# Performance work log

Measured on AMD Instinct MI355X. Metric: run time of the kernel, lower is better.

The kernel has to match this reference:

```python
import jax, jax.numpy as jnp
import numpy as np

B, S, D, H, FFN = 8, 1024, 1024, 16, 4096
DH = D // H  # per-head dim = 64
NEG = -1e9
EPS = 1e-5


def layer_norm(x):
    # F.layer_norm over last dim, no affine params (matches add_and_norm_dropout)
    mu = jnp.mean(x, axis=-1, keepdims=True)
    var = jnp.var(x, axis=-1, keepdims=True)
    return (x - mu) / jnp.sqrt(var + EPS)


def setup_inputs() -> dict:
    key = jax.random.key(0)
    ks = jax.random.split(key, 10)
    scale = 1.0 / np.sqrt(D)
    x = jax.random.normal(ks[0], (B, S, D), dtype=jnp.float32)
    real_lengths = jax.random.randint(ks[1], (B,), 1, S + 1)
    # per-head projection weights stacked: [H, D, DH] (nn.Linear(D, DH, bias=False) per head)
    Wq = jax.random.uniform(ks[2], (H, D, DH), jnp.float32, -scale, scale)
    Wk = jax.random.uniform(ks[3], (H, D, DH), jnp.float32, -scale, scale)
    Wv = jax.random.uniform(ks[4], (H, D, DH), jnp.float32, -scale, scale)
    Wo = jax.random.uniform(ks[5], (D, H * DH), jnp.float32, -scale, scale)  # Linear(H*DH, D, bias=False)
    W1 = jax.random.uniform(ks[6], (FFN, D), jnp.float32, -scale, scale)
    b1 = jax.random.uniform(ks[7], (FFN,), jnp.float32, -scale, scale)
    s2 = 1.0 / np.sqrt(FFN)
    W2 = jax.random.uniform(ks[8], (D, FFN), jnp.float32, -s2, s2)
    b2 = jax.random.uniform(ks[9], (D,), jnp.float32, -s2, s2)
    return {"x": x, "real_lengths": real_lengths, "Wq": Wq, "Wk": Wk, "Wv": Wv,
            "Wo": Wo, "W1": W1, "b1": b1, "W2": W2, "b2": b2}


def reference(x, real_lengths, Wq, Wk, Wv, Wo, W1, b1, W2, b2):
    b, s, d = x.shape
    # padding mask: True where key position >= real_length (masked out)
    key_pad = jnp.arange(s)[None, :] >= real_lengths[:, None]  # [B, S]

    # batched per-head projections (equivalent to the Python per-head loop)
    q = jnp.einsum('bsd,hde->bhse', x, Wq)
    k = jnp.einsum('bsd,hde->bhse', x, Wk)
    v = jnp.einsum('bsd,hde->bhse', x, Wv)

    scores = jnp.einsum('bhse,bhte->bhst', q, k) / jnp.sqrt(jnp.float32(DH))
    scores = jnp.where(key_pad[:, None, None, :], NEG, scores)
    attn = jax.nn.softmax(scores, axis=-1)
    heads = jnp.einsum('bhst,bhte->bhse', attn, v)       # [B,H,S,DH]
    concat = heads.transpose(0, 2, 1, 3).reshape(b, s, d)  # head concat
    attn_out = concat @ Wo.T

    x1 = layer_norm(x + attn_out)  # add & norm (eval: no dropout)

    ffn = jax.nn.relu(x1 @ W1.T + b1) @ W2.T + b2
    return layer_norm(x1 + ffn)
```

## Files before the change

### kernel.cpp

```cpp
#include <hip/hip_runtime.h>
#include <hip/hip_bf16.h>
#include <math.h>

#define B_ 8
#define S_ 1024
#define D_ 1024
#define H_ 16
#define DH_ 64
#define FFN_ 4096
#define NEG_ (-1e9f)
#define EPS_ 1e-5f

typedef float f32x4 __attribute__((ext_vector_type(4)));
typedef short bf16x8 __attribute__((ext_vector_type(8)));

__device__ __forceinline__ ushort f2b(float f) {
  __hip_bfloat16 h = __float2bfloat16(f);
  return *reinterpret_cast<ushort*>(&h);
}
__device__ __forceinline__ float b2f(ushort u) {
  return __uint_as_float((unsigned)u << 16);
}

__device__ __forceinline__ void gload16(const void* g, void* l) {
  auto* lp = (__attribute__((address_space(3))) unsigned*)(uintptr_t)(l);
  __builtin_amdgcn_global_load_lds(
      (const __attribute__((address_space(1))) unsigned*)g, lp, 16, 0, 0);
}

__device__ __forceinline__ void* swz_ptr(void* base, int row, int col) {
  int byte = (row << 7) + (col << 1);
  byte ^= (row & 7) << 4;
  return (char*)base + byte;
}
__device__ __forceinline__ void* swz256(void* base, int row, int col) {
  int byte = (row << 8) + (col << 1);
  byte ^= (row & 7) << 4;
  return (char*)base + byte;
}

#define BARR asm volatile("s_barrier" ::: "memory")
#define LGKM0                                         \
  do {                                                \
    asm volatile("s_waitcnt lgkmcnt(0)" ::: "memory"); \
    __builtin_amdgcn_sched_barrier(0);                \
  } while (0)

__global__ __launch_bounds__(256) void prep_k(
    const float* __restrict__ x, const float* __restrict__ Wq,
    const float* __restrict__ Wk, const float* __restrict__ Wv,
    const float* __restrict__ Wo, const float* __restrict__ W1,
    const float* __restrict__ W2, ushort* __restrict__ xbf,
    ushort* __restrict__ qkvw, ushort* __restrict__ wob,
    ushort* __restrict__ w1b, ushort* __restrict__ w2b) {
  const int blk = blockIdx.x, t = threadIdx.x;
  if (blk < 8192) {
    int i = blk * 256 + t;
    float4 v = ((const float4*)x)[i];
    ushort4 o;
    o.x = f2b(v.x); o.y = f2b(v.y); o.z = f2b(v.z); o.w = f2b(v.w);
    ((ushort4*)xbf)[i] = o;
  } else if (blk < 8192 + 12288) {
    int idx = (blk - 8192) * 256 + t;
    int k = idx & 1023, e = (idx >> 10) & 63;
    int h = (idx >> 16) & 15, which = idx >> 20;
    const float* W = (which == 0) ? Wq : (which == 1 ? Wk : Wv);
    float v = W[((size_t)h * D_ + k) * DH_ + e];
    qkvw[((size_t)which * 1024 + h * 64 + e) * 1024 + k] = f2b(v);
  } else if (blk < 8192 + 12288 + 1024) {
    int i = (blk - 8192 - 12288) * 256 + t;
    float4 v = ((const float4*)Wo)[i];
    ushort4 o;
    o.x = f2b(v.x); o.y = f2b(v.y); o.z = f2b(v.z); o.w = f2b(v.w);
    ((ushort4*)wob)[i] = o;
  } else if (blk < 8192 + 12288 + 1024 + 4096) {
    int i = (blk - 8192 - 12288 - 1024) * 256 + t;
    float4 v = ((const float4*)W1)[i];
    ushort4 o;
    o.x = f2b(v.x); o.y = f2b(v.y); o.z = f2b(v.z); o.w = f2b(v.w);
    ((ushort4*)w1b)[i] = o;
  } else {
    int i = (blk - 8192 - 12288 - 1024 - 4096) * 256 + t;
    float4 v = ((const float4*)W2)[i];
    ushort4 o;
    o.x = f2b(v.x); o.y = f2b(v.y); o.z = f2b(v.z); o.w = f2b(v.w);
    ((ushort4*)w2b)[i] = o;
  }
}

template <int BIAS, int RELU, int VSPLIT, int SPLITK>
__global__ __launch_bounds__(512, 2) void gemm8p(
    const ushort* __restrict__ A, const ushort* __restrict__ Bt,
    const float* __restrict__ bias, ushort* __restrict__ C,
    ushort* __restrict__ C2, int M, int N, int K) {
  __shared__ ushort lds[2][2][2][256 * 32];
  int bid = blockIdx.x;
  int nwg = gridDim.x;
  int kh2 = 0;
  if (SPLITK) {
    int hw = nwg >> 1;
    if (bid >= hw) { kh2 = 1; bid -= hw; }
    nwg = hw;
  }
  const int nbn = N >> 8;
  const int cpx = nwg >> 3;
  const int swz = (bid & 7) * cpx + (bid >> 3);
  const int bm = swz / nbn, bn = swz % nbn;
  const int Keff = SPLITK ? (K >> 1) : K;

  const int t = threadIdx.x;
  const int lane = t & 63, lr = lane & 15, lg = lane >> 4;
  const int wid = t >> 6, wr = wid >> 2, wc = wid & 3;
  const size_t Kb = (size_t)K * 2;
  const char* Ab = (const char*)A + ((size_t)(bm << 8)) * Kb +
                   (size_t)kh2 * Keff * 2;
  const char* Bb = (const char*)Bt + ((size_t)(bn << 8)) * Kb +
                   (size_t)kh2 * Keff * 2;
  const int NT = Keff >> 6;
  const int niter = NT >> 1;

  const int g0row = t >> 2;
  const int gsi = (t & 3) ^ ((g0row >> 2) & 3);
  auto STG = [&](int mat, int kh, int kt) {
    char* base = (char*)&lds[kt & 1][mat][kh][0];
    const char* gsrc = mat ? Bb : Ab;
#pragma unroll
    for (int j = 0; j < 2; j++) {
      int row = g0row + j * 128;
      const char* src = gsrc + (size_t)row * Kb +
                        (size_t)(kt * 64 + kh * 32) * 2 + gsi * 16;
      gload16(src, base + t * 16 + j * 8192);
    }
  };

  const int rg = (lg ^ ((lr >> 2) & 3)) << 3;
#define LDA(DST, BUF, KH, QM)                                            \
  _Pragma("unroll") for (int mm = 0; mm < 4; mm++) {                     \
    int row = wr * 128 + (QM)*64 + mm * 16 + lr;                         \
    DST[mm] = *(const bf16x8*)&lds[BUF][0][KH][row * 32 + rg];           \
  }
#define LDB(DST, BUF, KH)                                                \
  _Pragma("unroll") for (int nn = 0; nn < 4; nn++) {                     \
    int row = wc * 64 + nn * 16 + lr;                                    \
    DST[nn] = *(const bf16x8*)&lds[BUF][1][KH][row * 32 + rg];           \
  }
#define MFQ(QM, AS, BS)                                                  \
  do {                                                                   \
    __builtin_amdgcn_s_setprio(1);                                       \
    _Pragma("unroll") for (int mm = 0; mm < 4; mm++)                     \
        _Pragma("unroll") for (int nn = 0; nn < 4; nn++)                 \
            acc[(QM)*4 + mm][nn] = __builtin_amdgcn_mfma_f32_16x16x32_bf16( \
                AS[mm], BS[nn], acc[(QM)*4 + mm][nn], 0, 0, 0);          \
    __builtin_amdgcn_s_setprio(0);                                       \
  } while (0)

  f32x4 acc[8][4] = {};
  bf16x8 aS0[4], aS1[4], bS0[4], bS1[4];

  STG(0, 0, 0); STG(1, 0, 0); STG(0, 1, 0); STG(1, 1, 0);
  STG(0, 0, 1); STG(1, 0, 1);
  asm volatile("s_waitcnt vmcnt(4)" ::: "memory");
  BARR;

  for (int i = 0; i < niter; i++) {
    const int c1 = 2 * i + 1, c2 = 2 * i + 2, c3 = 2 * i + 3;
    LDA(aS0, 0, 0, 0); LDB(bS0, 0, 0); STG(0, 1, c1);
    BARR; LGKM0; MFQ(0, aS0, bS0); BARR;
    LDA(aS1, 0, 0, 1); STG(1, 1, c1);
    BARR; LGKM0; MFQ(1, aS1, bS0); BARR;
    LDA(aS0, 0, 1, 0); LDB(bS1, 0, 1);
    if (c2 < NT) STG(0, 0, c2);
    BARR; LGKM0; MFQ(0, aS0, bS1); BARR;
    LDA(aS1, 0, 1, 1);
    if (c2 < NT) STG(1, 0, c2);
    BARR; LGKM0; MFQ(1, aS1, bS1);
    if (i + 1 < niter)
      asm volatile("s_waitcnt vmcnt(4)" ::: "memory");
    else
      asm volatile("s_waitcnt vmcnt(0)" ::: "memory");
    BARR;
    LDA(aS0, 1, 0, 0); LDB(bS0, 1, 0);
    if (c2 < NT) STG(0, 1, c2);
    BARR; LGKM0; MFQ(0, aS0, bS0); BARR;
    LDA(aS1, 1, 0, 1);
    if (c2 < NT) STG(1, 1, c2);
    BARR; LGKM0; MFQ(1, aS1, bS0); BARR;
    LDA(aS0, 1, 1, 0); LDB(bS1, 1, 1);
    if (c3 < NT) STG(0, 0, c3);
    BARR; LGKM0; MFQ(0, aS0, bS1); BARR;
    LDA(aS1, 1, 1, 1);
    if (c3 < NT) STG(1, 0, c3);
    BARR; LGKM0; MFQ(1, aS1, bS1);
    asm volatile("s_waitcnt vmcnt(4)" ::: "memory");
    BARR;
  }
#undef LDA
#undef LDB
#undef MFQ

  ushort* Cout = (SPLITK && kh2) ? C2 : C;
  const int addb = BIAS && !(SPLITK && kh2);
  const int r0 = (bm << 8) + wr * 128 + lg * 4;
  const int c0 = (bn << 8) + wc * 64 + lr;
#pragma unroll
  for (int m = 0; m < 8; m++) {
#pragma unroll
    for (int n = 0; n < 4; n++) {
      int col = c0 + n * 16;
      float bv = addb ? bias[col] : 0.0f;
      if (VSPLIT && col >= 2048) {
        int row = r0 + m * 16;
        int hh = (col - 2048) >> 6, e = col & 63;
        ushort4 uv;
        uv.x = f2b(acc[m][n][0]); uv.y = f2b(acc[m][n][1]);
        uv.z = f2b(acc[m][n][2]); uv.w = f2b(acc[m][n][3]);
        *(ushort4*)&C2[((((size_t)(row >> 10) * 16 + hh) * 64 + e) << 10) +
                       (row & 1023)] = uv;
      } else {
#pragma unroll
        for (int q = 0; q < 4; q++) {
          int row = r0 + m * 16 + q;
          float v = acc[m][n][q] + bv;
          if (RELU) v = fmaxf(v, 0.0f);
          if (VSPLIT)
            Cout[(size_t)row * 2048 + col] = f2b(v);
          else
            Cout[(size_t)row * N + col] = f2b(v);
        }
      }
    }
  }
}

__global__ __launch_bounds__(256) void attention_mfma_k(
    const ushort* __restrict__ qk, const ushort* __restrict__ vT,
    const int* __restrict__ lens, ushort* __restrict__ concat) {
  __shared__ ushort Qs[64 * 64];
  __shared__ ushort Ks[128 * 64];
  __shared__ ushort Vt[64 * 128];
  __shared__ ushort Pl[4][16 * 128];
  const int blk = blockIdx.x;
  int lv[8];
#pragma unroll
  for (int j = 0; j < 8; j++) lv[j] = lens[j];
  const int rank = blk >> 8;
  int b = 0;
#pragma unroll
  for (int cand = 0; cand < 8; cand++) {
    int r = 0;
#pragma unroll
    for (int j = 0; j < 8; j++)
      r += (lv[j] > lv[cand]) || (lv[j] == lv[cand] && j < cand);
    if (r == rank) b = cand;
  }
  const int h = (blk >> 4) & 15, q0 = (blk & 15) << 6;
  const int t = threadIdx.x;
  const int lane = t & 63, w = t >> 6;
  const int lr = lane & 15, lg = lane >> 4;
  const int lg4 = lg * 4;
  const int len_b = lv[b];
  ushort* Plw = &Pl[w][0];
  const ushort* vbase = vT + ((size_t)(b * 16 + h) << 16);

#pragma unroll
  for (int i = 0; i < 4; i++) {
    int idx = t + i * 256;
    int r = idx >> 4, eq = idx & 15;
    const ushort* src =
        qk + ((size_t)(b * S_ + q0 + r)) * 2048 + h * 64 + eq * 4;
    *(ushort4*)swz_ptr(Qs, r, eq * 4) = *(const ushort4*)src;
  }
  __syncthreads();
  bf16x8 qf[2];
#pragma unroll
  for (int ds = 0; ds < 2; ds++)
    qf[ds] = *(const bf16x8*)swz_ptr(Qs, w * 16 + lr, lg * 8 + ds * 32);

  float mrun = -INFINITY, lrun = 0.f;
  f32x4 o[4] = {};

  ushort4 kreg[8], vreg[8];
  auto LOADT = [&](int j0) {
#pragma unroll
    for (int i = 0; i < 8; i++) {
      int idx = t + i * 256;
      int kr = idx >> 4, keq = idx & 15;
      kreg[i] = *(const ushort4*)(qk + ((size_t)(b * S_ + j0 + kr)) * 2048 +
                                  1024 + h * 64 + keq * 4);
      int vr = idx >> 5, vc = idx & 31;
      vreg[i] = *(const ushort4*)(vbase + (size_t)vr * 1024 + j0 + vc * 4);
    }
  };

  const int ntiles = (len_b + 127) >> 7;
  LOADT(0);
  for (int jt = 0; jt < ntiles; jt++) {
    const int j0 = jt << 7;
    __syncthreads();
#pragma unroll
    for (int i = 0; i < 8; i++) {
      int idx = t + i * 256;
      int kr = idx >> 4, keq = idx & 15;
      *(ushort4*)swz_ptr(Ks, kr, keq * 4) = kreg[i];
      int vr = idx >> 5, vc = idx & 31;
      *(ushort4*)swz256(Vt, vr, vc * 4) = vreg[i];
    }
    if (jt + 1 < ntiles) LOADT(j0 + 128);
    __syncthreads();

    f32x4 sacc[8];
    __builtin_amdgcn_s_setprio(1);
#pragma unroll
    for (int mb = 0; mb < 8; mb++) {
      sacc[mb] = (f32x4){0.f, 0.f, 0.f, 0.f};
#pragma unroll
      for (int ds = 0; ds < 2; ds++) {
        bf16x8 kf = *(const bf16x8*)swz_ptr(Ks, mb * 16 + lr, lg * 8 + ds * 32);
        sacc[mb] = __builtin_amdgcn_mfma_f32_16x16x32_bf16(kf, qf[ds], sacc[mb],
                                                           0, 0, 0);
      }
    }
    __builtin_amdgcn_s_setprio(0);

    float p[8][4];
    float pmax = -INFINITY;
#pragma unroll
    for (int mb = 0; mb < 8; mb++)
#pragma unroll
      for (int qi = 0; qi < 4; qi++) {
        float v = sacc[mb][qi] * 0.125f;
        if (j0 + mb * 16 + lg4 + qi >= len_b) v = NEG_;
        p[mb][qi] = v;
        pmax = fmaxf(pmax, v);
      }
    pmax = fmaxf(pmax, __shfl_xor(pmax, 16));
    pmax = fmaxf(pmax, __shfl_xor(pmax, 32));
    if (!__all(pmax - mrun <= 8.0f)) {
      float mnew = fmaxf(mrun, pmax);
      float sc = __expf(mrun - mnew);
      mrun = mnew;
      lrun *= sc;
#pragma unroll
      for (int qi = 0; qi < 4; qi++) {
        float scq = __shfl(sc, (lg << 4) + lg4 + qi);
#pragma unroll
        for (int dt = 0; dt < 4; dt++) o[dt][qi] *= scq;
      }
    }
    float rs = 0.f;
#pragma unroll
    for (int mb = 0; mb < 8; mb++)
#pragma unroll
      for (int qi = 0; qi < 4; qi++) {
        float e = __expf(p[mb][qi] - mrun);
        p[mb][qi] = e;
        rs += e;
      }
    rs += __shfl_xor(rs, 16);
    rs += __shfl_xor(rs, 32);
    lrun += rs;

#pragma unroll
    for (int mb = 0; mb < 8; mb++) {
      ushort2 w0, w1;
      w0.x = f2b(p[mb][0]); w0.y = f2b(p[mb][1]);
      w1.x = f2b(p[mb][2]); w1.y = f2b(p[mb][3]);
      *(ushort2*)swz256(Plw, lr, mb * 16 + lg4) = w0;
      *(ushort2*)swz256(Plw, lr, mb * 16 + lg4 + 2) = w1;
    }

    bf16x8 pf[4];
#pragma unroll
    for (int ks = 0; ks < 4; ks++)
      pf[ks] = *(const bf16x8*)swz256(Plw, lr, lg * 8 + ks * 32);
    __builtin_amdgcn_s_setprio(1);
#pragma unroll
    for (int dt = 0; dt < 4; dt++) {
#pragma unroll
      for (int ks = 0; ks < 4; ks++) {
        bf16x8 vf =
            *(const bf16x8*)swz256(Vt, dt * 16 + lr, ks * 32 + lg * 8);
        o[dt] = __builtin_amdgcn_mfma_f32_16x16x32_bf16(pf[ks], vf, o[dt],
                                                        0, 0, 0);
      }
    }
    __builtin_amdgcn_s_setprio(0);
  }

#pragma unroll
  for (int qi = 0; qi < 4; qi++) {
    float lq = __shfl(lrun, (lg << 4) + lg4 + qi);
    float inv = 1.0f / lq;
    size_t row = (size_t)(b * S_ + q0 + w * 16 + lg4 + qi);
#pragma unroll
    for (int dt = 0; dt < 4; dt++)
      concat[row * 1024 + h * 64 + dt * 16 + lr] = f2b(o[dt][qi] * inv);
  }
}

template <int WY, int WBF, int TWO, int ABF>
__global__ __launch_bounds__(256) void add_ln_k(const void* __restrict__ a,
                                                const ushort* __restrict__ r,
                                                const ushort* __restrict__ r2,
                                                float* __restrict__ y,
                                                ushort* __restrict__ yb) {
  const int row = blockIdx.x, t = threadIdx.x;
  float v[4];
  if (ABF) {
    const ushort4 av = ((const ushort4*)((const ushort*)a + (size_t)row * 1024))[t];
    v[0] = b2f(av.x); v[1] = b2f(av.y); v[2] = b2f(av.z); v[3] = b2f(av.w);
  } else {
    const float4 av = ((const float4*)((const float*)a + (size_t)row * 1024))[t];
    v[0] = av.x; v[1] = av.y; v[2] = av.z; v[3] = av.w;
  }
  const ushort4 rv = ((const ushort4*)(r + (size_t)row * 1024))[t];
  v[0] += b2f(rv.x); v[1] += b2f(rv.y); v[2] += b2f(rv.z); v[3] += b2f(rv.w);
  if (TWO) {
    const ushort4 r2v = ((const ushort4*)(r2 + (size_t)row * 1024))[t];
    v[0] += b2f(r2v.x); v[1] += b2f(r2v.y);
    v[2] += b2f(r2v.z); v[3] += b2f(r2v.w);
  }
  float s = v[0] + v[1] + v[2] + v[3];
  float q = v[0] * v[0] + v[1] * v[1] + v[2] * v[2] + v[3] * v[3];
#pragma unroll
  for (int off = 1; off < 64; off <<= 1) {
    s += __shfl_xor(s, off);
    q += __shfl_xor(q, off);
  }
  __shared__ float ss[4], sq[4];
  int wave = t >> 6, lane = t & 63;
  if (lane == 0) { ss[wave] = s; sq[wave] = q; }
  __syncthreads();
  s = ss[0] + ss[1] + ss[2] + ss[3];
  q = sq[0] + sq[1] + sq[2] + sq[3];
  float mean = s * (1.f / 1024.f);
  float var = q * (1.f / 1024.f) - mean * mean;
  float inv = 1.0f / sqrtf(var + EPS_);
  float4 yo;
  yo.x = (v[0] - mean) * inv; yo.y = (v[1] - mean) * inv;
  yo.z = (v[2] - mean) * inv; yo.w = (v[3] - mean) * inv;
  if (WY) ((float4*)(y + (size_t)row * 1024))[t] = yo;
  if (WBF) {
    ushort4 ob;
    ob.x = f2b(yo.x); ob.y = f2b(yo.y); ob.z = f2b(yo.z); ob.w = f2b(yo.w);
    ((ushort4*)(yb + (size_t)row * 1024))[t] = ob;
  }
}

extern "C" void kernel_launch(void* const* d_in, const int* in_sizes, int n_in,
                              void* d_out, int out_size, void* d_ws, size_t ws_size,
                              hipStream_t stream) {
  const float* x  = (const float*)d_in[0];
  const int* len  = (const int*)d_in[1];
  const float* Wq = (const float*)d_in[2];
  const float* Wk = (const float*)d_in[3];
  const float* Wv = (const float*)d_in[4];
  const float* Wo = (const float*)d_in[5];
  const float* W1 = (const float*)d_in[6];
  const float* b1 = (const float*)d_in[7];
  const float* W2 = (const float*)d_in[8];
  const float* b2 = (const float*)d_in[9];
  float* out = (float*)d_out;

  if (ws_size < (size_t)184 * 1024 * 1024) return;
  char* w = (char*)d_ws;
  ushort* xbf    = (ushort*)(w);
  ushort* qkvw   = (ushort*)(w + ((size_t)16 << 20));
  ushort* wob    = (ushort*)(w + ((size_t)22 << 20));
  ushort* w1b    = (ushort*)(w + ((size_t)24 << 20));
  ushort* w2b    = (ushort*)(w + ((size_t)32 << 20));
  ushort* qk2    = (ushort*)(w + ((size_t)40 << 20));
  ushort* vT     = (ushort*)(w + ((size_t)72 << 20));
  ushort* concat = (ushort*)(w + ((size_t)88 << 20));
  ushort* parta  = (ushort*)(w + ((size_t)104 << 20));
  ushort* partb  = (ushort*)(w + ((size_t)120 << 20));
  ushort* x1b    = (ushort*)(w + ((size_t)168 << 20));
  ushort* hidden = (ushort*)(w + ((size_t)40 << 20));

  prep_k<<<29696, 256, 0, stream>>>(x, Wq, Wk, Wv, Wo, W1, W2,
                                    xbf, qkvw, wob, w1b, w2b);

  gemm8p<0, 0, 1, 0><<<32 * 12, 512, 0, stream>>>(xbf, qkvw, nullptr, qk2,
                                                  vT, 8192, 3072, 1024);
  attention_mfma_k<<<2048, 256, 0, stream>>>(qk2, vT, len, concat);
  gemm8p<0, 0, 0, 1><<<256, 512, 0, stream>>>(concat, wob, nullptr, parta,
                                              partb, 8192, 1024, 1024);
  add_ln_k<0, 1, 1, 0><<<8192, 256, 0, stream>>>(x, parta, partb, nullptr,
                                                 x1b);
  gemm8p<1, 1, 0, 0><<<32 * 16, 512, 0, stream>>>(x1b, w1b, b1, hidden,
                                                  nullptr, 8192, 4096, 1024);
  gemm8p<1, 0, 0, 1><<<256, 512, 0, stream>>>(hidden, w2b, b2, parta,
                                              partb, 8192, 1024, 4096);
  add_ln_k<1, 0, 1, 1><<<8192, 256, 0, stream>>>(x1b, parta, partb, out,
                                                 nullptr);
}
```

Before: 358.4 us.

## Process 128 query rows per attention block to reuse each K/V tile twice

Each attention block now handles two 64-row query groups (128 rows), halving the grid to 1024 blocks. Each loaded K/V tile is reused for both groups, which halves global K/V traffic and the LDS staging work per query. Q is staged through the Ks buffer, so the separate Qs allocation is dropped. In exchange each thread holds twice the accumulator and softmax state, raising register pressure and lowering occupancy, and the smaller grid has coarser load balance across variable sequence lengths.

After: 382.4 us. 1.07x slower.

```diff
diff --git a/kernel.cpp b/kernel.cpp
--- a/kernel.cpp
+++ b/kernel.cpp
@@ -235,7 +235,6 @@
 __global__ __launch_bounds__(256) void attention_mfma_k(
     const ushort* __restrict__ qk, const ushort* __restrict__ vT,
     const int* __restrict__ lens, ushort* __restrict__ concat) {
-  __shared__ ushort Qs[64 * 64];
   __shared__ ushort Ks[128 * 64];
   __shared__ ushort Vt[64 * 128];
   __shared__ ushort Pl[4][16 * 128];
@@ -243,7 +242,7 @@
   int lv[8];
 #pragma unroll
   for (int j = 0; j < 8; j++) lv[j] = lens[j];
-  const int rank = blk >> 8;
+  const int rank = blk >> 7;
   int b = 0;
 #pragma unroll
   for (int cand = 0; cand < 8; cand++) {
@@ -253,7 +252,7 @@
       r += (lv[j] > lv[cand]) || (lv[j] == lv[cand] && j < cand);
     if (r == rank) b = cand;
   }
-  const int h = (blk >> 4) & 15, q0 = (blk & 15) << 6;
+  const int h = (blk >> 3) & 15, q0 = (blk & 7) << 7;
   const int t = threadIdx.x;
   const int lane = t & 63, w = t >> 6;
   const int lr = lane & 15, lg = lane >> 4;
@@ -263,21 +262,23 @@
   const ushort* vbase = vT + ((size_t)(b * 16 + h) << 16);
 
 #pragma unroll
-  for (int i = 0; i < 4; i++) {
+  for (int i = 0; i < 8; i++) {
     int idx = t + i * 256;
     int r = idx >> 4, eq = idx & 15;
     const ushort* src =
         qk + ((size_t)(b * S_ + q0 + r)) * 2048 + h * 64 + eq * 4;
-    *(ushort4*)swz_ptr(Qs, r, eq * 4) = *(const ushort4*)src;
+    *(ushort4*)swz_ptr(Ks, r, eq * 4) = *(const ushort4*)src;
   }
   __syncthreads();
-  bf16x8 qf[2];
-#pragma unroll
-  for (int ds = 0; ds < 2; ds++)
-    qf[ds] = *(const bf16x8*)swz_ptr(Qs, w * 16 + lr, lg * 8 + ds * 32);
-
-  float mrun = -INFINITY, lrun = 0.f;
-  f32x4 o[4] = {};
+  bf16x8 qfA[2], qfB[2];
+#pragma unroll
+  for (int ds = 0; ds < 2; ds++) {
+    qfA[ds] = *(const bf16x8*)swz_ptr(Ks, w * 16 + lr, lg * 8 + ds * 32);
+    qfB[ds] = *(const bf16x8*)swz_ptr(Ks, 64 + w * 16 + lr, lg * 8 + ds * 32);
+  }
+
+  float mA = -INFINITY, lA = 0.f, mB = -INFINITY, lB = 0.f;
+  f32x4 oA[4] = {}, oB[4] = {};
 
   ushort4 kreg[8], vreg[8];
   auto LOADT = [&](int j0) {
@@ -292,22 +293,8 @@
     }
   };
 
-  const int ntiles = (len_b + 127) >> 7;
-  LOADT(0);
-  for (int jt = 0; jt < ntiles; jt++) {
-    const int j0 = jt << 7;
-    __syncthreads();
-#pragma unroll
-    for (int i = 0; i < 8; i++) {
-      int idx = t + i * 256;
-      int kr = idx >> 4, keq = idx & 15;
-      *(ushort4*)swz_ptr(Ks, kr, keq * 4) = kreg[i];
-      int vr = idx >> 5, vc = idx & 31;
-      *(ushort4*)swz256(Vt, vr, vc * 4) = vreg[i];
-    }
-    if (jt + 1 < ntiles) LOADT(j0 + 128);
-    __syncthreads();
-
+  auto PROC = [&](const bf16x8 (&qf)[2], float& mrun, float& lrun,
+                  f32x4 (&o)[4], int j0) {
     f32x4 sacc[8];
     __builtin_amdgcn_s_setprio(1);
 #pragma unroll
@@ -385,16 +372,42 @@
       }
     }
     __builtin_amdgcn_s_setprio(0);
+  };
+
+  const int ntiles = (len_b + 127) >> 7;
+  LOADT(0);
+  for (int jt = 0; jt < ntiles; jt++) {
+    const int j0 = jt << 7;
+    __syncthreads();
+#pragma unroll
+    for (int i = 0; i < 8; i++) {
+      int idx = t + i * 256;
+      int kr = idx >> 4, keq = idx & 15;
+      *(ushort4*)swz_ptr(Ks, kr, keq * 4) = kreg[i];
+      int vr = idx >> 5, vc = idx & 31;
+      *(ushort4*)swz256(Vt, vr, vc * 4) = vreg[i];
+    }
+    if (jt + 1 < ntiles) LOADT(j0 + 128);
+    __syncthreads();
+
+    PROC(qfA, mA, lA, oA, j0);
+    PROC(qfB, mB, lB, oB, j0);
   }
 
 #pragma unroll
   for (int qi = 0; qi < 4; qi++) {
-    float lq = __shfl(lrun, (lg << 4) + lg4 + qi);
-    float inv = 1.0f / lq;
-    size_t row = (size_t)(b * S_ + q0 + w * 16 + lg4 + qi);
+    float lqA = __shfl(lA, (lg << 4) + lg4 + qi);
+    float invA = 1.0f / lqA;
+    size_t rowA = (size_t)(b * S_ + q0 + w * 16 + lg4 + qi);
 #pragma unroll
     for (int dt = 0; dt < 4; dt++)
-      concat[row * 1024 + h * 64 + dt * 16 + lr] = f2b(o[dt][qi] * inv);
+      concat[rowA * 1024 + h * 64 + dt * 16 + lr] = f2b(oA[dt][qi] * invA);
+    float lqB = __shfl(lB, (lg << 4) + lg4 + qi);
+    float invB = 1.0f / lqB;
+    size_t rowB = (size_t)(b * S_ + q0 + 64 + w * 16 + lg4 + qi);
+#pragma unroll
+    for (int dt = 0; dt < 4; dt++)
+      concat[rowB * 1024 + h * 64 + dt * 16 + lr] = f2b(oB[dt][qi] * invB);
   }
 }
 
@@ -482,7 +495,7 @@
 
   gemm8p<0, 0, 1, 0><<<32 * 12, 512, 0, stream>>>(xbf, qkvw, nullptr, qk2,
                                                   vT, 8192, 3072, 1024);
-  attention_mfma_k<<<2048, 256, 0, stream>>>(qk2, vT, len, concat);
+  attention_mfma_k<<<1024, 256, 0, stream>>>(qk2, vT, len, concat);
   gemm8p<0, 0, 0, 1><<<256, 512, 0, stream>>>(concat, wob, nullptr, parta,
                                               partb, 8192, 1024, 1024);
   add_ln_k<0, 1, 1, 0><<<8192, 256, 0, stream>>>(x, parta, partb, nullptr,
```
